# Performance work log

Hardware: AMD Instinct MI355X
Metric: run time of the kernel (lower is better)

Reference implementation:

```python
import jax, jax.numpy as jnp
import numpy as np

S, B, T = 512, 512, 64

def setup_inputs() -> dict:
    key = jax.random.key(0)
    k1, k2, k3, k4, k5 = jax.random.split(key, 5)
    feats = jax.random.normal(k1, (S, B, T), dtype=jnp.float32)
    # contiguous-prefix masks with variable lengths in [S//2, S]
    lengths = jax.random.randint(k2, (B,), S // 2, S + 1)
    mask = (jnp.arange(S)[None, :] < lengths[:, None]).astype(jnp.float32)  # (B,S)
    u = lambda k, shp: jax.random.uniform(k, shp, jnp.float32, -0.1, 0.1)
    return {
        "feats": feats,
        "mask": mask,
        "start_transitions": u(k3, (T,)),
        "end_transitions": u(k4, (T,)),
        "transitions": u(k5, (T, T)),
    }

def reference(feats, mask, start_transitions, end_transitions, transitions):
    # feats: (S, B, T) emissions; mask: (B, S) 1/0 float, left-aligned
    s, b, t = feats.shape
    maskT = mask.T  # (S, B)

    score0 = start_transitions[None, :] + feats[0]  # (B, T)

    def step(vscore, inp):
        emis, m = inp  # (B,T), (B,)
        # score[b, i, j] = vscore[b,i] + trans[i,j] + emis[b,j]
        scores = vscore[:, :, None] + transitions[None, :, :] + emis[:, None, :]
        best = jnp.max(scores, axis=1)                       # (B, T)
        bp = jnp.argmax(scores, axis=1).astype(jnp.int32)    # (B, T) backpointers
        m1 = m[:, None]
        new_v = best * m1 + vscore * (1.0 - m1)
        return new_v, bp * m1.astype(jnp.int32)

    final_v, history = jax.lax.scan(step, score0, (feats[1:], maskT[1:]))
    final_v = final_v + end_transitions[None, :]
    last_path = jnp.argmax(final_v, axis=1).astype(jnp.int32)  # (B,)

    # append pad row of zeros -> history: (S, B, T)
    history = jnp.concatenate([history, jnp.zeros((1, b, t), jnp.int32)], axis=0)

    # insert last_path at position (length - 1) for every tag column
    lengths = jnp.sum(mask, axis=1).astype(jnp.int32)  # (B,)
    hb = history.transpose(1, 0, 2)                    # (B, S, T)
    hb = hb.at[jnp.arange(b), lengths - 1, :].set(last_path[:, None])
    history = hb.transpose(1, 0, 2)                    # (S, B, T)

    # backtrack: decode_idx[i] = history[i][b, last_path[b]], i = S-2 .. 0
    def back(lp, h):
        new = jnp.take_along_axis(h, lp[:, None], axis=1)[:, 0]
        return new, new

    _, dec = jax.lax.scan(back, last_path, history[:-1], reverse=True)  # (S-1, B)
    # decode_idx[S-1] is uninitialized in the torch code; fill with argmax last tag
    decode = jnp.concatenate([dec, last_path[None, :]], axis=0)  # (S, B)
    return decode.T  # (B, S)
```

## Files before the change

kernel.cpp:

```cpp
#include <hip/hip_runtime.h>

#define SS 512
#define BB 512
#define TT 64
#define NTHREADS 256
#define FSTRIDE ((size_t)BB * TT)

template <int CTRL>
__device__ __forceinline__ float dppf(float x) {
    return __int_as_float(__builtin_amdgcn_mov_dpp(__float_as_int(x), CTRL, 0xF, 0xF, true));
}
template <int CTRL>
__device__ __forceinline__ int dppi(int x) {
    return __builtin_amdgcn_mov_dpp(x, CTRL, 0xF, 0xF, true);
}

__device__ __forceinline__ void barrier_lgkm() {
    asm volatile("s_waitcnt lgkmcnt(0)\n\ts_barrier" ::: "memory");
}

__global__ __launch_bounds__(NTHREADS, 2) void viterbi_fused(
    const float* __restrict__ feats,
    const float* __restrict__ mask,
    const float* __restrict__ startt,
    const float* __restrict__ endt,
    const float* __restrict__ trans,
    int* __restrict__ out)
{
    __shared__ float vbuf[2][TT];
    __shared__ unsigned char hist[SS - 1][TT];
    __shared__ float redbuf[4];
    __shared__ int lenSh;

    const int b   = blockIdx.x;
    const int tid = threadIdx.x;
    const int j   = tid >> 2;
    const int li  = tid & 3;
    const int base_i = li * 16;
    const int wid = tid >> 6;
    const int lane = tid & 63;

    float tcr[16];
#pragma unroll
    for (int k = 0; k < 16; ++k) tcr[k] = trans[(base_i + k) * TT + j];

    if (tid < TT) vbuf[0][tid] = startt[tid] + feats[(size_t)b * TT + tid];

    float msum = mask[b * SS + tid] + mask[b * SS + 256 + tid];
#pragma unroll
    for (int off = 1; off < 64; off <<= 1) msum += __shfl_xor(msum, off);
    if (lane == 0) redbuf[wid] = msum;
    __syncthreads();
    if (tid == 0) {
        float t = redbuf[0] + redbuf[1] + redbuf[2] + redbuf[3];
        lenSh = (int)(t + 0.5f);
    }
    __syncthreads();

    const int len = lenSh;
    int p = 0;

    const float* fb = feats + (size_t)b * TT + j;

    auto body = [&](float e, int s) {
        float v[16];
#pragma unroll
        for (int q = 0; q < 4; ++q) {
            float4 t4 = *(const float4*)&vbuf[p][base_i + q * 4];
            v[q * 4 + 0] = t4.x; v[q * 4 + 1] = t4.y;
            v[q * 4 + 2] = t4.z; v[q * 4 + 3] = t4.w;
        }
        float sc[16];
#pragma unroll
        for (int k = 0; k < 16; ++k) sc[k] = (v[k] + tcr[k]) + e;

        float c0 = sc[0];  int x0 = 0;
        float c1 = sc[4];  int x1 = 4;
        float c2 = sc[8];  int x2 = 8;
        float c3 = sc[12]; int x3 = 12;
#pragma unroll
        for (int k = 1; k < 4; ++k) {
            if (sc[k]      > c0) { c0 = sc[k];      x0 = k; }
            if (sc[4 + k]  > c1) { c1 = sc[4 + k];  x1 = 4 + k; }
            if (sc[8 + k]  > c2) { c2 = sc[8 + k];  x2 = 8 + k; }
            if (sc[12 + k] > c3) { c3 = sc[12 + k]; x3 = 12 + k; }
        }
        if (c1 > c0) { c0 = c1; x0 = x1; }
        if (c3 > c2) { c2 = c3; x2 = x3; }
        if (c2 > c0) { c0 = c2; x0 = x2; }
        float best = c0;
        int   bi   = base_i + x0;

        {
            float ov = dppf<0xB1>(best);
            int   oi = dppi<0xB1>(bi);
            if (ov > best || (ov == best && oi < bi)) { best = ov; bi = oi; }
            ov = dppf<0x4E>(best);
            oi = dppi<0x4E>(bi);
            if (ov > best || (ov == best && oi < bi)) { best = ov; bi = oi; }
        }

        if (li == 0) {
            vbuf[p ^ 1][j] = best;
            hist[s - 1][j] = (unsigned char)bi;
        }
        barrier_lgkm();
        p ^= 1;
    };

    float ec[8], en[8];
#pragma unroll
    for (int u = 0; u < 8; ++u) {
        int sn = 1 + u; if (sn > SS - 1) sn = SS - 1;
        ec[u] = fb[(size_t)sn * FSTRIDE];
    }

    int s = 1;
    while (s + 8 <= len) {
#pragma unroll
        for (int u = 0; u < 8; ++u) {
            int sn = s + 8 + u; if (sn > SS - 1) sn = SS - 1;
            en[u] = fb[(size_t)sn * FSTRIDE];
        }
#pragma unroll
        for (int u = 0; u < 8; ++u) body(ec[u], s + u);
#pragma unroll
        for (int u = 0; u < 8; ++u) ec[u] = en[u];
        s += 8;
    }
#pragma unroll
    for (int u = 0; u < 7; ++u) {
        if (s + u < len) body(ec[u], s + u);
    }

    if (tid < TT) {
        float fv = vbuf[p][tid] + endt[tid];
        int bix = tid;
#pragma unroll
        for (int off = 1; off < 64; off <<= 1) {
            float ov = __shfl_xor(fv, off);
            int   oi = __shfl_xor(bix, off);
            if (ov > fv || (ov == fv && oi < bix)) { fv = ov; bix = oi; }
        }
        if (tid == 0) {
            int* ob = out + (size_t)b * SS;
            int cur = bix;
            ob[SS - 1] = cur;
            ob[len - 1] = cur;
            for (int s2 = len - 2; s2 >= 0; --s2) {
                cur = hist[s2][cur];
                ob[s2] = cur;
            }
        }
    }

    for (int s2 = len + tid; s2 < SS - 1; s2 += NTHREADS)
        out[(size_t)b * SS + s2] = 0;
}

extern "C" void kernel_launch(void* const* d_in, const int* in_sizes, int n_in,
                              void* d_out, int out_size, void* d_ws, size_t ws_size,
                              hipStream_t stream) {
    const float* feats  = (const float*)d_in[0];
    const float* mask   = (const float*)d_in[1];
    const float* startt = (const float*)d_in[2];
    const float* endt   = (const float*)d_in[3];
    const float* trans  = (const float*)d_in[4];
    int* out = (int*)d_out;

    viterbi_fused<<<dim3(BB), dim3(NTHREADS), 0, stream>>>(
        feats, mask, startt, endt, trans, out);
}
```

Before: 258.2 us.

## Split each tag across two threads with packed adds and max-then-index argmax

Halves the block to 128 threads so each tag's 64 predecessors are split over two lanes of 32 candidates each instead of four lanes of 16. Scores are computed with packed v_pk_add_f32, and the argmax takes an fmax tree for the value followed by an equality search for the smallest matching index, instead of a compare-and-select chain. The cross-lane reduction needs only one DPP swap. The aim is to shorten the serial per-timestep chain and make the per-step barrier cheaper with fewer waves, at the cost of more work per thread and fewer threads to hide latency.

```diff
diff --git a/kernel.cpp b/kernel.cpp
--- a/kernel.cpp
+++ b/kernel.cpp
@@ -3,23 +3,29 @@
 #define SS 512
 #define BB 512
 #define TT 64
-#define NTHREADS 256
+#define NTHREADS 128
 #define FSTRIDE ((size_t)BB * TT)
 
-template <int CTRL>
-__device__ __forceinline__ float dppf(float x) {
-    return __int_as_float(__builtin_amdgcn_mov_dpp(__float_as_int(x), CTRL, 0xF, 0xF, true));
+typedef float float2v __attribute__((ext_vector_type(2)));
+
+__device__ __forceinline__ float2v pk_add(float2v a, float2v b) {
+    float2v d;
+    asm("v_pk_add_f32 %0, %1, %2" : "=v"(d) : "v"(a), "v"(b));
+    return d;
 }
-template <int CTRL>
-__device__ __forceinline__ int dppi(int x) {
-    return __builtin_amdgcn_mov_dpp(x, CTRL, 0xF, 0xF, true);
+
+__device__ __forceinline__ float dppf_x1(float x) {
+    return __int_as_float(__builtin_amdgcn_mov_dpp(__float_as_int(x), 0xB1, 0xF, 0xF, true));
+}
+__device__ __forceinline__ int dppi_x1(int x) {
+    return __builtin_amdgcn_mov_dpp(x, 0xB1, 0xF, 0xF, true);
 }
 
 __device__ __forceinline__ void barrier_lgkm() {
     asm volatile("s_waitcnt lgkmcnt(0)\n\ts_barrier" ::: "memory");
 }
 
-__global__ __launch_bounds__(NTHREADS, 2) void viterbi_fused(
+__global__ __launch_bounds__(NTHREADS, 1) void viterbi_fused(
     const float* __restrict__ feats,
     const float* __restrict__ mask,
     const float* __restrict__ startt,
@@ -29,32 +35,34 @@
 {
     __shared__ float vbuf[2][TT];
     __shared__ unsigned char hist[SS - 1][TT];
-    __shared__ float redbuf[4];
+    __shared__ float redbuf[2];
     __shared__ int lenSh;
 
     const int b   = blockIdx.x;
     const int tid = threadIdx.x;
-    const int j   = tid >> 2;
-    const int li  = tid & 3;
-    const int base_i = li * 16;
+    const int j   = tid >> 1;
+    const int li  = tid & 1;
+    const int base_i = li * 32;
     const int wid = tid >> 6;
-    const int lane = tid & 63;
 
-    float tcr[16];
+    float2v tc2[16];
 #pragma unroll
-    for (int k = 0; k < 16; ++k) tcr[k] = trans[(base_i + k) * TT + j];
+    for (int q = 0; q < 16; ++q) {
+        float2v t;
+        t.x = trans[(base_i + 2 * q) * TT + j];
+        t.y = trans[(base_i + 2 * q + 1) * TT + j];
+        tc2[q] = t;
+    }
 
     if (tid < TT) vbuf[0][tid] = startt[tid] + feats[(size_t)b * TT + tid];
 
-    float msum = mask[b * SS + tid] + mask[b * SS + 256 + tid];
+    float msum = mask[b * SS + tid] + mask[b * SS + 128 + tid]
+               + mask[b * SS + 256 + tid] + mask[b * SS + 384 + tid];
 #pragma unroll
     for (int off = 1; off < 64; off <<= 1) msum += __shfl_xor(msum, off);
-    if (lane == 0) redbuf[wid] = msum;
+    if ((tid & 63) == 0) redbuf[wid] = msum;
     __syncthreads();
-    if (tid == 0) {
-        float t = redbuf[0] + redbuf[1] + redbuf[2] + redbuf[3];
-        lenSh = (int)(t + 0.5f);
-    }
+    if (tid == 0) lenSh = (int)(redbuf[0] + redbuf[1] + 0.5f);
     __syncthreads();
 
     const int len = lenSh;
@@ -63,46 +71,53 @@
     const float* fb = feats + (size_t)b * TT + j;
 
     auto body = [&](float e, int s) {
-        float v[16];
+        float2v vv[16];
 #pragma unroll
-        for (int q = 0; q < 4; ++q) {
+        for (int q = 0; q < 8; ++q) {
             float4 t4 = *(const float4*)&vbuf[p][base_i + q * 4];
-            v[q * 4 + 0] = t4.x; v[q * 4 + 1] = t4.y;
-            v[q * 4 + 2] = t4.z; v[q * 4 + 3] = t4.w;
+            float2v a; a.x = t4.x; a.y = t4.y; vv[2 * q]     = a;
+            float2v c; c.x = t4.z; c.y = t4.w; vv[2 * q + 1] = c;
         }
-        float sc[16];
+        float2v ee; ee.x = e; ee.y = e;
+
+        float sc[32];
 #pragma unroll
-        for (int k = 0; k < 16; ++k) sc[k] = (v[k] + tcr[k]) + e;
+        for (int q = 0; q < 16; ++q) {
+            float2v r = pk_add(pk_add(vv[q], tc2[q]), ee);
+            sc[2 * q]     = r.x;
+            sc[2 * q + 1] = r.y;
+        }
 
-        float c0 = sc[0];  int x0 = 0;
-        float c1 = sc[4];  int x1 = 4;
-        float c2 = sc[8];  int x2 = 8;
-        float c3 = sc[12]; int x3 = 12;
+        float t[11];
 #pragma unroll
-        for (int k = 1; k < 4; ++k) {
-            if (sc[k]      > c0) { c0 = sc[k];      x0 = k; }
-            if (sc[4 + k]  > c1) { c1 = sc[4 + k];  x1 = 4 + k; }
-            if (sc[8 + k]  > c2) { c2 = sc[8 + k];  x2 = 8 + k; }
-            if (sc[12 + k] > c3) { c3 = sc[12 + k]; x3 = 12 + k; }
+        for (int k = 0; k < 10; ++k)
+            t[k] = fmaxf(fmaxf(sc[3 * k], sc[3 * k + 1]), sc[3 * k + 2]);
+        t[10] = fmaxf(sc[30], sc[31]);
+        float u0 = fmaxf(fmaxf(t[0], t[1]), t[2]);
+        float u1 = fmaxf(fmaxf(t[3], t[4]), t[5]);
+        float u2 = fmaxf(fmaxf(t[6], t[7]), t[8]);
+        float u3 = fmaxf(t[9], t[10]);
+        float best = fmaxf(fmaxf(fmaxf(u0, u1), u2), u3);
+
+        best = fmaxf(best, dppf_x1(best));
+
+        int ci = 9999;
+#pragma unroll
+        for (int c = 0; c < 4; ++c) {
+            int cc = 9999;
+#pragma unroll
+            for (int k = 7; k >= 0; --k) {
+                int kk = c * 8 + k;
+                if (sc[kk] == best) cc = kk;
+            }
+            ci = min(ci, cc);
         }
-        if (c1 > c0) { c0 = c1; x0 = x1; }
-        if (c3 > c2) { c2 = c3; x2 = x3; }
-        if (c2 > c0) { c0 = c2; x0 = x2; }
-        float best = c0;
-        int   bi   = base_i + x0;
-
-        {
-            float ov = dppf<0xB1>(best);
-            int   oi = dppi<0xB1>(bi);
-            if (ov > best || (ov == best && oi < bi)) { best = ov; bi = oi; }
-            ov = dppf<0x4E>(best);
-            oi = dppi<0x4E>(bi);
-            if (ov > best || (ov == best && oi < bi)) { best = ov; bi = oi; }
-        }
+        int gi = base_i + ci;
+        gi = min(gi, dppi_x1(gi));
 
         if (li == 0) {
             vbuf[p ^ 1][j] = best;
-            hist[s - 1][j] = (unsigned char)bi;
+            hist[s - 1][j] = (unsigned char)gi;
         }
         barrier_lgkm();
         p ^= 1;
```

Result: slower. 305.0 us (+18.1%).

## Process two batch rows per block, sharing one barrier per step

Applied to the files above, without the earlier changes.

Each block now runs the Viterbi recursion for two sequences (b and b+256) together. Both max/argmax bodies execute between a single barrier per time step, which halves the barrier count per sequence and interleaves two independent dependency chains to hide latency. The grid shrinks to 256 blocks, uses dynamic LDS for two history buffers, and the two backtracks plus zero-fill run on different wavefronts. The risks are fewer blocks to cover the GPU's compute units and steps sized by the longer of the two lengths.

```diff
diff --git a/kernel.cpp b/kernel.cpp
--- a/kernel.cpp
+++ b/kernel.cpp
@@ -4,7 +4,10 @@
 #define BB 512
 #define TT 64
 #define NTHREADS 256
+#define NBLK (BB / 2)
 #define FSTRIDE ((size_t)BB * TT)
+#define HISTBYTES ((SS - 1) * TT)
+#define DYNLDS (1024 + 2 * HISTBYTES)
 
 template <int CTRL>
 __device__ __forceinline__ float dppf(float x) {
@@ -19,7 +22,7 @@
     asm volatile("s_waitcnt lgkmcnt(0)\n\ts_barrier" ::: "memory");
 }
 
-__global__ __launch_bounds__(NTHREADS, 2) void viterbi_fused(
+__global__ __launch_bounds__(NTHREADS) void viterbi_pair(
     const float* __restrict__ feats,
     const float* __restrict__ mask,
     const float* __restrict__ startt,
@@ -27,12 +30,17 @@
     const float* __restrict__ trans,
     int* __restrict__ out)
 {
-    __shared__ float vbuf[2][TT];
-    __shared__ unsigned char hist[SS - 1][TT];
-    __shared__ float redbuf[4];
-    __shared__ int lenSh;
-
-    const int b   = blockIdx.x;
+    extern __shared__ __align__(16) char smem[];
+    float (*vbufA)[TT] = (float (*)[TT])(smem);
+    float (*vbufB)[TT] = (float (*)[TT])(smem + 512);
+    unsigned char* histA = (unsigned char*)(smem + 1024);
+    unsigned char* histB = histA + HISTBYTES;
+
+    __shared__ float redA[4], redB[4];
+    __shared__ int lenShA, lenShB;
+
+    const int bA  = blockIdx.x;
+    const int bB  = blockIdx.x + NBLK;
     const int tid = threadIdx.x;
     const int j   = tid >> 2;
     const int li  = tid & 3;
@@ -44,25 +52,35 @@
 #pragma unroll
     for (int k = 0; k < 16; ++k) tcr[k] = trans[(base_i + k) * TT + j];
 
-    if (tid < TT) vbuf[0][tid] = startt[tid] + feats[(size_t)b * TT + tid];
-
-    float msum = mask[b * SS + tid] + mask[b * SS + 256 + tid];
-#pragma unroll
-    for (int off = 1; off < 64; off <<= 1) msum += __shfl_xor(msum, off);
-    if (lane == 0) redbuf[wid] = msum;
+    if (tid < TT) {
+        vbufA[0][tid] = startt[tid] + feats[(size_t)bA * TT + tid];
+        vbufB[0][tid] = startt[tid] + feats[(size_t)bB * TT + tid];
+    }
+
+    float msA = mask[bA * SS + tid] + mask[bA * SS + 256 + tid];
+    float msB = mask[bB * SS + tid] + mask[bB * SS + 256 + tid];
+#pragma unroll
+    for (int off = 1; off < 64; off <<= 1) {
+        msA += __shfl_xor(msA, off);
+        msB += __shfl_xor(msB, off);
+    }
+    if (lane == 0) { redA[wid] = msA; redB[wid] = msB; }
     __syncthreads();
     if (tid == 0) {
-        float t = redbuf[0] + redbuf[1] + redbuf[2] + redbuf[3];
-        lenSh = (int)(t + 0.5f);
+        lenShA = (int)(redA[0] + redA[1] + redA[2] + redA[3] + 0.5f);
+        lenShB = (int)(redB[0] + redB[1] + redB[2] + redB[3] + 0.5f);
     }
     __syncthreads();
 
-    const int len = lenSh;
-    int p = 0;
-
-    const float* fb = feats + (size_t)b * TT + j;
-
-    auto body = [&](float e, int s) {
+    const int lenA = lenShA;
+    const int lenB = lenShB;
+    const int smax = (lenA > lenB) ? lenA : lenB;
+    int pA = 0, pB = 0;
+
+    const float* fbA = feats + (size_t)bA * TT + j;
+    const float* fbB = feats + (size_t)bB * TT + j;
+
+    auto body = [&](float (*vbuf)[TT], unsigned char* hist, int p, float e, int s) {
         float v[16];
 #pragma unroll
         for (int q = 0; q < 4; ++q) {
@@ -102,60 +120,96 @@
 
         if (li == 0) {
             vbuf[p ^ 1][j] = best;
-            hist[s - 1][j] = (unsigned char)bi;
-        }
-        barrier_lgkm();
-        p ^= 1;
+            hist[(s - 1) * TT + j] = (unsigned char)bi;
+        }
     };
 
-    float ec[8], en[8];
+    float ecA[8], enA[8], ecB[8], enB[8];
 #pragma unroll
     for (int u = 0; u < 8; ++u) {
         int sn = 1 + u; if (sn > SS - 1) sn = SS - 1;
-        ec[u] = fb[(size_t)sn * FSTRIDE];
+        ecA[u] = fbA[(size_t)sn * FSTRIDE];
+        ecB[u] = fbB[(size_t)sn * FSTRIDE];
     }
 
     int s = 1;
-    while (s + 8 <= len) {
+    while (s + 8 <= smax) {
 #pragma unroll
         for (int u = 0; u < 8; ++u) {
             int sn = s + 8 + u; if (sn > SS - 1) sn = SS - 1;
-            en[u] = fb[(size_t)sn * FSTRIDE];
-        }
-#pragma unroll
-        for (int u = 0; u < 8; ++u) body(ec[u], s + u);
-#pragma unroll
-        for (int u = 0; u < 8; ++u) ec[u] = en[u];
+            enA[u] = fbA[(size_t)sn * FSTRIDE];
+            enB[u] = fbB[(size_t)sn * FSTRIDE];
+        }
+#pragma unroll
+        for (int u = 0; u < 8; ++u) {
+            const bool rA = (s + u < lenA), rB = (s + u < lenB);
+            if (rA) body(vbufA, histA, pA, ecA[u], s + u);
+            if (rB) body(vbufB, histB, pB, ecB[u], s + u);
+            barrier_lgkm();
+            if (rA) pA ^= 1;
+            if (rB) pB ^= 1;
+        }
+#pragma unroll
+        for (int u = 0; u < 8; ++u) { ecA[u] = enA[u]; ecB[u] = enB[u]; }
         s += 8;
     }
 #pragma unroll
     for (int u = 0; u < 7; ++u) {
-        if (s + u < len) body(ec[u], s + u);
+        if (s + u < smax) {
+            const bool rA = (s + u < lenA), rB = (s + u < lenB);
+            if (rA) body(vbufA, histA, pA, ecA[u], s + u);
+            if (rB) body(vbufB, histB, pB, ecB[u], s + u);
+            barrier_lgkm();
+            if (rA) pA ^= 1;
+            if (rB) pB ^= 1;
+        }
     }
 
     if (tid < TT) {
-        float fv = vbuf[p][tid] + endt[tid];
-        int bix = tid;
+        float fv = vbufA[pA][lane] + endt[lane];
+        int bix = lane;
 #pragma unroll
         for (int off = 1; off < 64; off <<= 1) {
             float ov = __shfl_xor(fv, off);
             int   oi = __shfl_xor(bix, off);
             if (ov > fv || (ov == fv && oi < bix)) { fv = ov; bix = oi; }
         }
-        if (tid == 0) {
-            int* ob = out + (size_t)b * SS;
+        if (lane == 0) {
+            int* ob = out + (size_t)bA * SS;
             int cur = bix;
             ob[SS - 1] = cur;
-            ob[len - 1] = cur;
-            for (int s2 = len - 2; s2 >= 0; --s2) {
-                cur = hist[s2][cur];
+            ob[lenA - 1] = cur;
+            for (int s2 = lenA - 2; s2 >= 0; --s2) {
+                cur = histA[s2 * TT + cur];
                 ob[s2] = cur;
             }
         }
-    }
-
-    for (int s2 = len + tid; s2 < SS - 1; s2 += NTHREADS)
-        out[(size_t)b * SS + s2] = 0;
+    } else if (tid < 2 * TT) {
+        float fv = vbufB[pB][lane] + endt[lane];
+        int bix = lane;
+#pragma unroll
+        for (int off = 1; off < 64; off <<= 1) {
+            float ov = __shfl_xor(fv, off);
+            int   oi = __shfl_xor(bix, off);
+            if (ov > fv || (ov == fv && oi < bix)) { fv = ov; bix = oi; }
+        }
+        if (lane == 0) {
+            int* ob = out + (size_t)bB * SS;
+            int cur = bix;
+            ob[SS - 1] = cur;
+            ob[lenB - 1] = cur;
+            for (int s2 = lenB - 2; s2 >= 0; --s2) {
+                cur = histB[s2 * TT + cur];
+                ob[s2] = cur;
+            }
+        }
+    } else if (tid < 3 * TT) {
+        for (int s2 = lenA + lane; s2 < SS - 1; s2 += TT)
+            out[(size_t)bA * SS + s2] = 0;
+    } else {
+        for (int s2 = lenB + lane; s2 < SS - 1; s2 += TT)
+            out[(size_t)bB * SS + s2] = 0;
+    }
 }
 
 extern "C" void kernel_launch(void* const* d_in, const int* in_sizes, int n_in,
@@ -168,6 +222,9 @@
     const float* trans  = (const float*)d_in[4];
     int* out = (int*)d_out;
 
-    viterbi_fused<<<dim3(BB), dim3(NTHREADS), 0, stream>>>(
+    hipFuncSetAttribute((const void*)viterbi_pair,
+                        hipFuncAttributeMaxDynamicSharedMemorySize, DYNLDS);
+
+    viterbi_pair<<<dim3(NBLK), dim3(NTHREADS), DYNLDS, stream>>>(
         feats, mask, startt, endt, trans, out);
 }
```

Measured after the change: 401.9 us. +55.7%, slower.
